# Optimization experiments

Measured on AMD Instinct MI355X. Metric: run time of the kernel, lower is better.

Reference implementation:

```python
import jax, jax.numpy as jnp
import numpy as np
from jax import lax

B, N, FIN, T, K, FC, FT = 8, 2048, 3, 12, 3, 64, 64


def _conv2d(x, w, b, pad):
    # x [B,C,N,T], w [O,I,1,kw], NCHW conv
    y = lax.conv_general_dilated(x, w, (1, 1), pad,
                                 dimension_numbers=('NCHW', 'OIHW', 'NCHW'))
    return y + b[None, :, None, None]


def _spatial_att(h, W, a, alpha, concat):
    # GAT-style dense attention. h [B,N,Fin], W [Fin,D], a [2D,1]
    D = W.shape[1]
    Wh = h @ W                                             # [B,N,D]
    e = jax.nn.leaky_relu(Wh @ a[:D] + jnp.swapaxes(Wh @ a[D:], 1, 2), alpha)  # [B,N,N]
    att = jax.nn.softmax(jax.nn.sigmoid(e), axis=1)        # softmax over dim=1 (as in torch)
    hp = jnp.einsum('bij,bjd->bid', att, Wh)
    return jax.nn.elu(hp) if concat else hp


def setup_inputs() -> dict:
    key = jax.random.key(0)
    ks = jax.random.split(key, 24)
    rnd = lambda i, shape, scale=1.0: (jax.random.normal(ks[i], shape, dtype=jnp.float32) * scale)
    FTm = FC * T  # 768 spatial-attention feature dim
    D = FTm // 2
    return {
        'x': rnd(0, (B, N, FIN, T)),
        'cheb': rnd(1, (K, N, N), 1.0 / np.sqrt(N)),
        'Gamma': rnd(2, (K, FIN, FC), 1.0 / np.sqrt(FIN)),
        'W_heads': rnd(3, (2, FTm, D), 1.0 / np.sqrt(FTm)),
        'a_heads': rnd(4, (2, 2 * D, 1), 1.0 / np.sqrt(2 * D)),
        'W_out': rnd(5, (FTm, FTm), 1.0 / np.sqrt(FTm)),
        'a_out': rnd(6, (2 * FTm, 1), 1.0 / np.sqrt(2 * FTm)),
        'U1': rnd(7, (FT, FT), 1.0 / np.sqrt(FT)),
        'U2': rnd(8, (FT,), 1.0 / np.sqrt(FT)),
        'U3': rnd(9, (FT,), 1.0 / np.sqrt(FT)),
        'be': rnd(10, (1, T, T), 0.1),
        'Ve': rnd(11, (T, T), 1.0 / np.sqrt(T)),
        'time_w': rnd(12, (FT, FC, 1, 3), 1.0 / np.sqrt(3 * FC)),
        'time_b': rnd(13, (FT,), 0.01),
        'res_w': rnd(14, (FT, FIN, 1, 1), 1.0 / np.sqrt(FIN)),
        'res_b': rnd(15, (FT,), 0.01),
        'back_w': rnd(16, (FT, FC, 1, 3), 1.0 / np.sqrt(3 * FC)),
        'back_b': rnd(17, (FT,), 0.01),
        'fore_w': rnd(18, (FT, FC, 1, 3), 1.0 / np.sqrt(3 * FC)),
        'fore_b': rnd(19, (FT,), 0.01),
        'ln_g': jnp.ones((FT,), jnp.float32),
        'ln_b': jnp.zeros((FT,), jnp.float32),
    }


def reference(x, cheb, Gamma, W_heads, a_heads, W_out, a_out, U1, U2, U3, be, Ve,
              time_w, time_b, res_w, res_b, back_w, back_b, fore_w, fore_b, ln_g, ln_b):
    b, n, fin, t = x.shape
    k_ = cheb.shape[0]
    fc = Gamma.shape[2]
    # ChebNetII interpolation coefficients T_k(x_j), x_j = cos((j+0.5)pi/K) -> [j,k]
    jj = np.arange(k_)
    cxj = jnp.asarray(np.cos(np.outer((jj + 0.5) * np.pi / k_, np.arange(k_))), x.dtype)
    lhs = jnp.einsum('jio,jk->kio', Gamma, cxj)                         # [K,Fin,Fc]
    rhs = jnp.einsum('bnit,knm->kbmit', x, cheb)                        # [K,B,N,Fin,T]
    spatial_gcn = jax.nn.relu((2.0 / (k_ + 1)) * jnp.einsum('kbmit,kio->bmot', rhs, lhs))  # [B,N,Fc,T]

    # Spatial transformer: 2 GAT heads + output attention
    h = spatial_gcn.reshape(b, n, fc * t)
    heads = jax.vmap(lambda W, a: _spatial_att(h, W, a, 0.1, True))(W_heads, a_heads)  # [H,B,N,D]
    hcat = jnp.transpose(heads, (1, 2, 0, 3)).reshape(b, n, -1)
    gcn_SAt = jax.nn.relu(_spatial_att(hcat, W_out, a_out, 0.1, False)).reshape(b, n, fc, t)

    # Temporal conv (1x3, pad 1)
    tc = _conv2d(jnp.transpose(gcn_SAt, (0, 2, 1, 3)), time_w, time_b, ((0, 0), (1, 1)))
    tc = jnp.transpose(tc, (0, 2, 1, 3))                                # [B,N,Ft,T]

    # Temporal attention
    lhs_t = jnp.einsum('bnft,fg,g->btn', tc, U1, U2)                    # [B,T,N]
    rhs_t = jnp.einsum('f,bnft->bnt', U3, tc)                           # [B,N,T]
    prod = jnp.einsum('bsn,bnt->bst', lhs_t, rhs_t)                     # [B,T,T]
    E = jnp.einsum('is,bst->bit', Ve, jax.nn.sigmoid(prod + be))
    E = jax.nn.softmax(E, axis=1)
    tcn = jnp.einsum('bnft,bts->bnfs', tc, E)                           # [B,N,Ft,T]

    # Residual (1x1 conv) + LayerNorm over channel dim
    x_res = _conv2d(jnp.transpose(x, (0, 2, 1, 3)), res_w, res_b, ((0, 0), (0, 0)))
    x_res = jnp.transpose(x_res, (0, 2, 1, 3))                          # [B,N,Ft,T]
    z = jnp.transpose(jax.nn.relu(x_res + tcn), (0, 3, 1, 2))           # [B,T,N,Ft]
    mu = z.mean(-1, keepdims=True)
    var = z.var(-1, keepdims=True)
    z = (z - mu) / jnp.sqrt(var + 1e-5) * ln_g + ln_b
    result = jnp.transpose(z, (0, 2, 3, 1))                             # [B,N,Ft,T]

    rp = jnp.transpose(result, (0, 2, 1, 3))
    backcast = jnp.transpose(_conv2d(rp, back_w, back_b, ((0, 0), (1, 1))), (0, 2, 1, 3))
    forecast = jnp.transpose(_conv2d(rp, fore_w, fore_b, ((0, 0), (1, 1))), (0, 2, 1, 3))
    return (backcast, forecast)
```

## Files before the change

kernel.cpp:

```cpp
#include <hip/hip_runtime.h>


typedef unsigned short u16;
typedef __bf16 bf16x8 __attribute__((ext_vector_type(8)));
typedef float f32x4 __attribute__((ext_vector_type(4)));
typedef u16 u16x8 __attribute__((ext_vector_type(8)));

__device__ __forceinline__ u16 f2b(float f) {
  union { float f; unsigned u; } v; v.f = f;
  unsigned u = v.u;
  u = u + 0x7FFFu + ((u >> 16) & 1u);
  return (u16)(u >> 16);
}
__device__ __forceinline__ float b2f(u16 h) {
  union { unsigned u; float f; } v; v.u = ((unsigned)h) << 16; return v.f;
}
__device__ __forceinline__ float qfun(float x) {
  float e = x > 0.f ? x : 0.1f * x;
  float s = __builtin_amdgcn_rcpf(1.f + __expf(-e));
  return __expf(s);
}

template <int N> __device__ __forceinline__ void waitvm() {
  if constexpr (N == 0)      asm volatile("s_waitcnt vmcnt(0)" ::: "memory");
  else if constexpr (N == 4) asm volatile("s_waitcnt vmcnt(4)" ::: "memory");
  else                       asm volatile("s_waitcnt vmcnt(6)" ::: "memory");
}
__device__ __forceinline__ void rawbar() { asm volatile("s_barrier" ::: "memory"); }

#define GLOAD16(g, l) __builtin_amdgcn_global_load_lds( \
    (__attribute__((address_space(1))) void*)(g),       \
    (__attribute__((address_space(3))) void*)(l), 16, 0, 0)

constexpr size_t OFF_LHS     = 0x0;
constexpr size_t OFF_U1U2    = 0x1000;
constexpr size_t OFF_BIASBIG = 0x1100;
constexpr size_t OFF_FH      = 0x3000;
constexpr size_t OFF_GH      = 0x23000;
constexpr size_t OFF_RDH     = 0x43000;
constexpr size_t OFF_FO      = 0x63000;
constexpr size_t OFF_GO      = 0x73000;
constexpr size_t OFF_RDO     = 0x83000;
constexpr size_t OFF_LHST    = 0x93000;
constexpr size_t OFF_RHST    = 0x153000;
constexpr size_t OFF_PROD    = 0x213000;
constexpr size_t OFF_E       = 0x215000;
constexpr size_t OFF_WCATT   = 0x220000;
constexpr size_t OFF_WOUTT   = 0x340000;
constexpr size_t OFF_WTBIG   = 0x460000;
constexpr size_t OFF_XCOLT   = 0x580000;
constexpr size_t OFF_CHEBT   = 0x700000;
constexpr size_t OFF_C1      = 0x1F00000;
constexpr size_t OFF_H       = 0x4300000;
constexpr size_t OFF_P       = 0x700000;
constexpr size_t OFF_WHCATT  = 0x5B00000;
constexpr size_t OFF_HCAT    = 0x7300000;
constexpr size_t OFF_WHOUTT  = 0x5B00000;
constexpr size_t OFF_GCNB    = 0x7300000;
constexpr size_t OFF_WBFBIG  = 0x8B00000;
constexpr size_t OFF_TCS     = 0x700000;
constexpr size_t OFF_RESULTB = 0x3700000;
constexpr size_t WS_NEEDED   = 0x8D40000;

struct GemmP {
  const u16* A; const u16* BT;
  long sA, sB;
  int K, lda, ldb;
  int swz, splitK;
  float* Cf; long sCf; int ldcf;
  u16* Cb;  long sCb; int ldcb;
  u16* CbT; int ldcT; long sCbT;
  const float* bias;
  float* outB; float* outF;
};

template <int EPI, int WN>
__global__ __launch_bounds__(256, (WN == 1 ? 3 : 2)) void gemm_bf16(GemmP p) {
  constexpr int BUFU  = (WN == 1) ? 8192 : 12288;
  constexpr int SMEMU = 3 * BUFU;
  constexpr int LPW   = (WN == 1) ? 4 : 6;
  __shared__ u16 smem[SMEMU];
  const int tid  = threadIdx.x;
  const int lane = tid & 63;
  const int wid  = tid >> 6;
  const int wm = wid >> 1, wn = wid & 1;
  const int z = blockIdx.z;

  long m0, n0;
  if (p.swz) {
    int nT = gridDim.x;
    int nwg = nT * gridDim.y;
    int lin = blockIdx.x + nT * blockIdx.y;
    int q = nwg >> 3;
    int swz = (lin & 7) * q + (lin >> 3);
    m0 = (long)(swz / nT) * 128;
    n0 = (long)(swz % nT) * (128 * WN);
  } else {
    m0 = (long)blockIdx.y * 128;
    n0 = (long)blockIdx.x * (128 * WN);
  }

  const int K = p.K;
  long aBase, bBase;
  if (p.splitK) {
    int kz = z >> 2, ch = z & 3;
    aBase = (long)kz * p.sA + (long)ch * 512;
    bBase = (long)ch * 512;
  } else {
    aBase = (long)z * p.sA;
    bBase = (long)z * p.sB;
  }
  const u16* Ab = p.A + aBase + m0 * p.lda;
  const u16* Bb = p.BT + bBase + n0 * p.ldb;

  const int sk = (((lane & 3) ^ ((lane >> 3) & 3))) * 8;
  const u16* aP0 = Ab + (long)(wid * 32 + (lane >> 2)) * p.lda + sk;
  const u16* aP1 = aP0 + (long)16 * p.lda;
  const u16* bP0 = Bb + (long)(wid * 32 * WN + (lane >> 2)) * p.ldb + sk;
  const u16* bP1 = bP0 + (long)16 * p.ldb;
  const u16* bP2 = bP0 + (long)32 * p.ldb;
  const u16* bP3 = bP0 + (long)48 * p.ldb;
  const int aslot = wid * 1024;
  const int bslot = 4096 + wid * (WN == 1 ? 1024 : 2048);

  auto STAGE = [&](int s, int bi) {
    long ko = (long)s * 32;
    u16* base = smem + bi * BUFU;
    GLOAD16(aP0 + ko, base + aslot);
    GLOAD16(aP1 + ko, base + aslot + 512);
    GLOAD16(bP0 + ko, base + bslot);
    GLOAD16(bP1 + ko, base + bslot + 512);
    if constexpr (WN == 2) {
      GLOAD16(bP2 + ko, base + bslot + 1024);
      GLOAD16(bP3 + ko, base + bslot + 1536);
    }
  };

  f32x4 acc[4][4 * WN];
  f32x4 zero = {0.f, 0.f, 0.f, 0.f};
#pragma unroll
  for (int i = 0; i < 4; ++i)
#pragma unroll
    for (int j = 0; j < 4 * WN; ++j) acc[i][j] = zero;

  const int xorc = (lane >> 1) & 3;
  const int aoff = (wm * 64 + (lane & 15)) * 32 + ((lane >> 4) ^ xorc) * 8;
  const int boff = 4096 + (wn * 64 * WN + (lane & 15)) * 32 + ((lane >> 4) ^ xorc) * 8;

  const int nsteps = K >> 5;

  STAGE(0, 0);
  STAGE(1, 1);
  waitvm<LPW>();
  rawbar();

  int cur = 0;
  for (int i = 0; i < nsteps; ++i) {
    const u16* buf = smem + cur * BUFU;
    bf16x8 av[4], bv[4 * WN];
#pragma unroll
    for (int mi = 0; mi < 4; ++mi) av[mi] = *(const bf16x8*)&buf[aoff + mi * 512];
#pragma unroll
    for (int ni = 0; ni < 4 * WN; ++ni) bv[ni] = *(const bf16x8*)&buf[boff + ni * 512];
#pragma unroll
    for (int mi = 0; mi < 4; ++mi)
#pragma unroll
      for (int ni = 0; ni < 4 * WN; ++ni)
        acc[mi][ni] = __builtin_amdgcn_mfma_f32_16x16x32_bf16(av[mi], bv[ni], acc[mi][ni], 0, 0, 0);
    if (i + 1 < nsteps) {
      if (i + 2 < nsteps) {
        STAGE(i + 2, cur == 0 ? 2 : cur - 1);
        waitvm<LPW>();
      } else {
        waitvm<0>();
      }
      rawbar();
    }
    cur = (cur == 2) ? 0 : cur + 1;
  }
  __syncthreads();

  if constexpr (EPI == 1) {
#pragma unroll
    for (int h = 0; h < 2; ++h) {
      if (h == 1) __syncthreads();
      if (WN == 1 || wn == h) {
#pragma unroll
        for (int mi = 0; mi < 4; ++mi)
#pragma unroll
          for (int ni = 0; ni < 4 * WN; ++ni) {
            int cl = (WN == 1 ? wn * 64 : 0) + ni * 16 + (lane & 15);
            int mlb = wm * 64 + mi * 16 + ((lane >> 4) << 2);
#pragma unroll
            for (int r = 0; r < 4; ++r)
              smem[cl * 136 + mlb + r] = f2b(acc[mi][ni][r]);
          }
      }
      __syncthreads();
      int c = tid >> 1, half = tid & 1;
      long bat = m0 >> 11;
      u16* dst = p.CbT + bat * p.sCbT + (long)(n0 + h * 128 + c) * p.ldcT +
                 (m0 & 2047) + half * 64;
      const u16* srcp = &smem[c * 136 + half * 64];
#pragma unroll
      for (int j = 0; j < 64; j += 8)
        *(u16x8*)(dst + j) = *(const u16x8*)(srcp + j);
      if (WN == 1) break;
    }
    return;
  }

  if constexpr (EPI == 7) {
    const int q = lane >> 4, g4 = (lane >> 2) & 3, j = lane & 3;
    const int back = ((int)n0 < 768);
    float* obase = (back ? p.outB : p.outF) - (back ? 0 : 768);
#pragma unroll
    for (int mi = 0; mi < 4; ++mi) {
      long rb0 = m0 + wm * 64 + mi * 16 + q * 4;
#pragma unroll
      for (int ni = 0; ni < 4 * WN; ++ni) {
        int cb = (int)n0 + wn * 64 * WN + ni * 16 + g4 * 4;
        f32x4 v = acc[mi][ni];
        float bsv = p.bias[cb + j];
        v[0] += bsv; v[1] += bsv; v[2] += bsv; v[3] += bsv;
#pragma unroll
        for (int d = 1; d <= 2; d <<= 1) {
          f32x4 t;
#pragma unroll
          for (int b = 0; b < 4; ++b) t[b] = __shfl_xor(v[b ^ d], d, 64);
#pragma unroll
          for (int b = 0; b < 4; ++b) if ((lane ^ b) & d) v[b] = t[b];
        }
        *(f32x4*)(obase + (rb0 + j) * 768 + cb) = v;
      }
    }
    return;
  }

#pragma unroll
  for (int mi = 0; mi < 4; ++mi) {
    long rb0 = m0 + wm * 64 + mi * 16 + ((lane >> 4) << 2);
#pragma unroll
    for (int ni = 0; ni < 4 * WN; ++ni) {
      int col = (int)n0 + wn * 64 * WN + ni * 16 + (lane & 15);
#pragma unroll
      for (int r = 0; r < 4; ++r) {
        float v = acc[mi][ni][r];
        long row = rb0 + r;
        if constexpr (EPI == 2) {
          float e = v > 0.f ? v : expm1f(v);
          p.Cb[(long)z * p.sCb + row * p.ldcb + col] = f2b(e);
        } else if constexpr (EPI == 6) {
          p.Cb[row * 768 + col] = f2b(v + p.bias[col & 63]);
        } else if constexpr (EPI == 9) {
          p.Cb[(long)z * p.sCb + row * p.ldcb + col] = f2b(v);
        } else {
          p.Cb[(long)z * p.sCb + row * p.ldcb + col] = f2b(fmaxf(v, 0.f));
        }
      }
    }
  }
}

__global__ void k_prep(const float* Gamma, const float* U1, const float* U2,
                       const float* back_b, const float* fore_b,
                       float* lhs, float* u1u2, float* biasBig) {
  int o = threadIdx.x;
  if (o < 64) {
    const float cx[3][3] = {{1.f, 0.86602540378443871f, 0.5f},
                            {1.f, 6.123233995736766e-17f, -1.f},
                            {1.f, -0.86602540378443871f, 0.5f}};
    for (int k = 0; k < 3; ++k)
      for (int i = 0; i < 3; ++i) {
        float s = 0;
        for (int j = 0; j < 3; ++j) s += Gamma[(j * 3 + i) * 64 + o] * cx[j][k];
        lhs[(k * 3 + i) * 64 + o] = s;
      }
    float s = 0;
    for (int g = 0; g < 64; ++g) s += U1[o * 64 + g] * U2[g];
    u1u2[o] = s;
    for (int t = 0; t < 12; ++t) {
      biasBig[o * 12 + t] = back_b[o];
      biasBig[768 + o * 12 + t] = fore_b[o];
    }
  }
}

__global__ void k_convert(const float* W_heads, const float* W_out, const float* time_w,
                          const float* back_w, const float* fore_w, const float* xg,
                          u16* WcatT, u16* WoutT, u16* WtBig, u16* WbfBig, u16* xcolT) {
  const int N1 = 589824, NT = 589824, NBF = 1179648, N5 = 786432;
  const int TOT = 2 * N1 + NT + NBF + N5;
  for (int o = blockIdx.x * 256 + threadIdx.x; o < TOT; o += gridDim.x * 256) {
    if (o < N1) {
      int dcol = o / 768, kk = o % 768;
      int hd = dcol / 384, d = dcol % 384;
      WcatT[o] = f2b(W_heads[((long)hd * 768 + kk) * 384 + d]);
    } else if (o < 2 * N1) {
      int o2 = o - N1; int dcol = o2 / 768, kk = o2 % 768;
      WoutT[o2] = f2b(W_out[kk * 768 + dcol]);
    } else if (o < 2 * N1 + NT) {
      int o3 = o - 2 * N1; int col = o3 / 768, kk = o3 % 768;
      int t = col >> 6, ft = col & 63, fc = kk / 12, tau = kk % 12;
      int r = tau - t + 1;
      WtBig[o3] = f2b((r >= 0 && r < 3) ? time_w[ft * 192 + fc * 3 + r] : 0.f);
    } else if (o < 2 * N1 + NT + NBF) {
      int o4 = o - 2 * N1 - NT; int col = o4 / 768, kk = o4 % 768;
      int rem = (col < 768) ? col : col - 768;
      int c = rem / 12, tt = rem % 12;
      int fc = kk / 12, tau = kk % 12; int r = tau - tt + 1;
      const float* wsrc = (col < 768) ? back_w : fore_w;
      WbfBig[o4] = f2b((r >= 0 && r < 3) ? wsrc[c * 192 + fc * 3 + r] : 0.f);
    } else {
      int o5 = o - 2 * N1 - NT - NBF; int c = o5 / 2048, n = o5 % 2048;
      float v = 0.f;
      if (c < 288) {
        int b = c / 36, r2 = c % 36, i = r2 / 12, t = r2 % 12;
        v = xg[(long)(b * 2048 + n) * 36 + i * 12 + t];
      }
      xcolT[o5] = f2b(v);
    }
  }
}

__global__ void k_chebT(const float* cheb, u16* chebT) {
  __shared__ float ts[32][33];
  int n0 = blockIdx.x * 32, m0 = blockIdx.y * 32, k = blockIdx.z;
  int c = threadIdx.x & 31, rq = threadIdx.x >> 5;
  const long base = (long)k * 2048 * 2048;
  for (int q = 0; q < 4; ++q) {
    int n = n0 + rq + q * 8;
    ts[rq + q * 8][c] = cheb[base + (long)n * 2048 + m0 + c];
  }
  __syncthreads();
  for (int q = 0; q < 4; ++q) {
    int m = m0 + rq + q * 8;
    chebT[base + (long)m * 2048 + n0 + c] = f2b(ts[c][rq + q * 8]);
  }
}

__global__ __launch_bounds__(256) void k_h(const u16* C1, const float* lhs, u16* h) {
  int bn = blockIdx.x; int b = bn >> 11, n = bn & 2047;
  int tid = threadIdx.x;
  __shared__ float c1s[108], ls[576];
  if (tid < 108) {
    int kk = tid / 12, t = tid % 12; int k = kk / 3, i = kk % 3;
    float s = 0;
#pragma unroll
    for (int ch = 0; ch < 4; ++ch)
      s += b2f(C1[((long)(k * 4 + ch) * 2048 + n) * 384 + b * 36 + i * 12 + t]);
    c1s[tid] = s;
  }
  for (int s = tid; s < 576; s += 256) ls[s] = lhs[s];
  __syncthreads();
  for (int q = 0; q < 3; ++q) {
    int idx = tid + q * 256; int o = idx / 12, t = idx % 12;
    float s = 0;
#pragma unroll
    for (int kk = 0; kk < 9; ++kk) s += c1s[kk * 12 + t] * ls[kk * 64 + o];
    s *= 0.5f;
    if (s < 0.f) s = 0.f;
    h[(long)bn * 768 + idx] = f2b(s);
  }
}

__global__ __launch_bounds__(256) void k_fg(const u16* WhT, int dOff, int Dlen,
                                            const float* aF, const float* aG,
                                            float* fOut, float* gOut) {
  int b = blockIdx.y;
  int i = blockIdx.x * 256 + threadIdx.x;
  __shared__ float af[768], ag[768];
  for (int s = threadIdx.x; s < Dlen; s += 256) { af[s] = aF[s]; ag[s] = aG[s]; }
  __syncthreads();
  const u16* wp = WhT + ((long)b * 768 + dOff) * 2048 + i;
  float fs = 0, gs = 0;
  for (int d = 0; d < Dlen; ++d) {
    float w = b2f(wp[(long)d * 2048]);
    fs += w * af[d]; gs += w * ag[d];
  }
  fOut[b * 2048 + i] = fs;
  gOut[b * 2048 + i] = gs;
}

__global__ __launch_bounds__(256) void k_denom(const float* f, const float* g, float* rd) {
  int b = blockIdx.y;
  int jl = threadIdx.x & 63, ch = threadIdx.x >> 6;
  int j = blockIdx.x * 64 + jl;
  __shared__ float fl[2048];
  __shared__ float red[256];
  for (int s = threadIdx.x; s < 2048; s += 256) fl[s] = f[b * 2048 + s];
  __syncthreads();
  float gj = g[b * 2048 + j];
  float acc = 0;
  for (int i = ch * 512; i < ch * 512 + 512; ++i) acc += qfun(fl[i] + gj);
  red[threadIdx.x] = acc;
  __syncthreads();
  if (ch == 0) {
    float s = red[jl] + red[jl + 64] + red[jl + 128] + red[jl + 192];
    rd[b * 2048 + j] = 1.f / s;
  }
}

__global__ __launch_bounds__(256) void k_P(const float* f, const float* g,
                                           const float* rd, u16* P) {
  int j = blockIdx.x * 256 + threadIdx.x;
  int i0 = blockIdx.y * 16;
  int b = blockIdx.z;
  __shared__ float fl[16];
  if (threadIdx.x < 16) fl[threadIdx.x] = f[b * 2048 + i0 + threadIdx.x];
  __syncthreads();
  float gj = g[b * 2048 + j], rj = rd[b * 2048 + j];
  u16* Pp = P + ((long)b * 2048 + i0) * 2048 + j;
#pragma unroll
  for (int ii = 0; ii < 16; ++ii) Pp[(long)ii * 2048] = f2b(qfun(fl[ii] + gj) * rj);
}

__global__ void k_temporal(const u16* tc, const float* u1u2, const float* U3g,
                           float* lhs_t, float* rhs_t) {
  __shared__ float uu[64], u3[64];
  int tid = threadIdx.x;
  if (tid < 64) { uu[tid] = u1u2[tid]; u3[tid] = U3g[tid]; }
  __syncthreads();
  int gid = blockIdx.x * 256 + tid;
  const u16* p = tc + (long)gid * 64;
  float s1 = 0, s2 = 0;
#pragma unroll
  for (int c = 0; c < 8; ++c) {
    u16x8 vv = *(const u16x8*)(p + c * 8);
#pragma unroll
    for (int j = 0; j < 8; ++j) {
      float v = b2f(vv[j]);
      s1 += v * uu[c * 8 + j]; s2 += v * u3[c * 8 + j];
    }
  }
  int t = gid % 12; long bn = gid / 12;
  int b = (int)(bn >> 11);
  lhs_t[((long)b * 12 + t) * 2048 + (int)(bn & 2047)] = s1;
  rhs_t[gid] = s2;
}

__global__ void k_prod(const float* lhs_t, const float* rhs_t, float* prod) {
  int bi = blockIdx.x;
  int b = bi / 144; int r = bi % 144; int s = r / 12; int u = r % 12;
  int tid = threadIdx.x;
  float acc = 0;
  const float* lp = lhs_t + ((long)b * 12 + s) * 2048;
  const float* rp = rhs_t + (long)b * 2048 * 12 + u;
  for (int n = tid; n < 2048; n += 256) acc += lp[n] * rp[n * 12];
  __shared__ float red[256];
  red[tid] = acc; __syncthreads();
  for (int st = 128; st > 0; st >>= 1) {
    if (tid < st) red[tid] += red[tid + st];
    __syncthreads();
  }
  if (tid == 0) prod[bi] = red[0];
}

__global__ void k_E(const float* prod, const float* be, const float* Ve, float* E) {
  int b = blockIdx.x; int tid = threadIdx.x;
  __shared__ float S0[144], E1[144], mx[12], dn[12];
  if (tid < 144) {
    float v = prod[b * 144 + tid] + be[tid];
    S0[tid] = 1.f / (1.f + __expf(-v));
  }
  __syncthreads();
  if (tid < 144) {
    int i = tid / 12, t = tid % 12;
    float a = 0;
    for (int s = 0; s < 12; ++s) a += Ve[i * 12 + s] * S0[s * 12 + t];
    E1[tid] = a;
  }
  __syncthreads();
  if (tid < 12) {
    float m = -1e30f;
    for (int i = 0; i < 12; ++i) m = fmaxf(m, E1[i * 12 + tid]);
    float d = 0;
    for (int i = 0; i < 12; ++i) d += __expf(E1[i * 12 + tid] - m);
    mx[tid] = m; dn[tid] = d;
  }
  __syncthreads();
  if (tid < 144) {
    int t = tid % 12;
    E[b * 144 + tid] = __expf(E1[tid] - mx[t]) / dn[t];
  }
}

__global__ __launch_bounds__(256) void k_res_ln(const u16* tc, const float* E,
                                                const float* xg, const float* res_w,
                                                const float* res_b, const float* ln_g,
                                                const float* ln_b, u16* result) {
  int bn = blockIdx.x; int b = bn >> 11;
  int tid = threadIdx.x;
  __shared__ float tcb[768], Eb[144], xl[36], rw[192], rb[64], lg[64], lb[64], zl[768], mu[12], rs[12];
  for (int s = tid; s < 768; s += 256) tcb[s] = b2f(tc[(long)bn * 768 + s]);
  if (tid < 144) Eb[tid] = E[b * 144 + tid];
  if (tid < 36) xl[tid] = xg[(long)bn * 36 + tid];
  if (tid >= 64 && tid < 256) { int q = tid - 64; if (q < 192) rw[q] = res_w[q]; }
  if (tid < 64) { rb[tid] = res_b[tid]; lg[tid] = ln_g[tid]; lb[tid] = ln_b[tid]; }
  __syncthreads();
  float z[3];
#pragma unroll
  for (int q = 0; q < 3; ++q) {
    int idx = tid + q * 256; int f = idx / 12, s = idx % 12;
    float tcn = 0;
#pragma unroll
    for (int t = 0; t < 12; ++t) tcn += tcb[t * 64 + f] * Eb[t * 12 + s];
    float xr = rb[f];
#pragma unroll
    for (int i = 0; i < 3; ++i) xr += rw[f * 3 + i] * xl[i * 12 + s];
    float v = xr + tcn;
    v = v > 0.f ? v : 0.f;
    z[q] = v; zl[idx] = v;
  }
  __syncthreads();
  if (tid < 12) {
    float m = 0, m2 = 0;
    for (int f = 0; f < 64; ++f) { float v = zl[f * 12 + tid]; m += v; m2 += v * v; }
    m *= (1.f / 64.f); m2 *= (1.f / 64.f);
    mu[tid] = m;
    float var = m2 - m * m;
    rs[tid] = rsqrtf((var > 0.f ? var : 0.f) + 1e-5f);
  }
  __syncthreads();
#pragma unroll
  for (int q = 0; q < 3; ++q) {
    int idx = tid + q * 256; int f = idx / 12, s = idx % 12;
    result[(long)bn * 768 + idx] = f2b((z[q] - mu[s]) * rs[s] * lg[f] + lb[f]);
  }
}

__global__ void k_sentinel(float* out, long n) {
  long i = (long)blockIdx.x * 256 + threadIdx.x;
  if (i < n) out[i] = 12345.0f;
}

extern "C" void kernel_launch(void* const* d_in, const int* in_sizes, int n_in,
                              void* d_out, int out_size, void* d_ws, size_t ws_size,
                              hipStream_t stream) {
  (void)in_sizes; (void)n_in;
  const float* x       = (const float*)d_in[0];
  const float* cheb    = (const float*)d_in[1];
  const float* Gamma   = (const float*)d_in[2];
  const float* W_heads = (const float*)d_in[3];
  const float* a_heads = (const float*)d_in[4];
  const float* W_out   = (const float*)d_in[5];
  const float* a_out   = (const float*)d_in[6];
  const float* U1      = (const float*)d_in[7];
  const float* U2      = (const float*)d_in[8];
  const float* U3      = (const float*)d_in[9];
  const float* be      = (const float*)d_in[10];
  const float* Ve      = (const float*)d_in[11];
  const float* time_w  = (const float*)d_in[12];
  const float* time_b  = (const float*)d_in[13];
  const float* res_w   = (const float*)d_in[14];
  const float* res_b   = (const float*)d_in[15];
  const float* back_w  = (const float*)d_in[16];
  const float* back_b  = (const float*)d_in[17];
  const float* fore_w  = (const float*)d_in[18];
  const float* fore_b  = (const float*)d_in[19];
  const float* ln_g    = (const float*)d_in[20];
  const float* ln_b    = (const float*)d_in[21];
  float* out = (float*)d_out;

  if (ws_size < WS_NEEDED) {
    k_sentinel<<<(out_size + 255) / 256, 256, 0, stream>>>(out, out_size);
    return;
  }

  char* ws = (char*)d_ws;
  float* lhs     = (float*)(ws + OFF_LHS);
  float* u1u2    = (float*)(ws + OFF_U1U2);
  float* biasBig = (float*)(ws + OFF_BIASBIG);
  float* fH      = (float*)(ws + OFF_FH);
  float* gH      = (float*)(ws + OFF_GH);
  float* rdH     = (float*)(ws + OFF_RDH);
  float* fO      = (float*)(ws + OFF_FO);
  float* gO      = (float*)(ws + OFF_GO);
  float* rdO     = (float*)(ws + OFF_RDO);
  float* lhs_t   = (float*)(ws + OFF_LHST);
  float* rhs_t   = (float*)(ws + OFF_RHST);
  float* prod    = (float*)(ws + OFF_PROD);
  float* Ebuf    = (float*)(ws + OFF_E);
  u16* WcatT   = (u16*)(ws + OFF_WCATT);
  u16* WoutT   = (u16*)(ws + OFF_WOUTT);
  u16* WtBig   = (u16*)(ws + OFF_WTBIG);
  u16* WbfBig  = (u16*)(ws + OFF_WBFBIG);
  u16* xcolT   = (u16*)(ws + OFF_XCOLT);
  u16* chebT   = (u16*)(ws + OFF_CHEBT);
  u16* C1      = (u16*)(ws + OFF_C1);
  u16* hbuf    = (u16*)(ws + OFF_H);
  u16* Pbuf    = (u16*)(ws + OFF_P);
  u16* WhcatT  = (u16*)(ws + OFF_WHCATT);
  u16* hcat    = (u16*)(ws + OFF_HCAT);
  u16* WhoutT  = (u16*)(ws + OFF_WHOUTT);
  u16* gcnB    = (u16*)(ws + OFF_GCNB);
  u16* tcsB    = (u16*)(ws + OFF_TCS);
  u16* resultB = (u16*)(ws + OFF_RESULTB);

  k_prep<<<1, 64, 0, stream>>>(Gamma, U1, U2, back_b, fore_b, lhs, u1u2, biasBig);
  k_convert<<<2048, 256, 0, stream>>>(W_heads, W_out, time_w, back_w, fore_w, x,
                                      WcatT, WoutT, WtBig, WbfBig, xcolT);
  k_chebT<<<dim3(64, 64, 3), 256, 0, stream>>>(cheb, chebT);

  {
    GemmP p{}; p.A = chebT; p.BT = xcolT; p.sA = 2048L * 2048; p.sB = 0;
    p.K = 512; p.lda = 2048; p.ldb = 2048; p.splitK = 1; p.swz = 1;
    p.Cb = C1; p.sCb = 2048L * 384; p.ldcb = 384;
    gemm_bf16<9, 1><<<dim3(3, 16, 12), 256, 0, stream>>>(p);
  }
  k_h<<<16384, 256, 0, stream>>>(C1, lhs, hbuf);

  {
    GemmP p{}; p.A = hbuf; p.BT = WcatT; p.sA = 0; p.sB = 0;
    p.K = 768; p.lda = 768; p.ldb = 768; p.swz = 1;
    p.CbT = WhcatT; p.ldcT = 2048; p.sCbT = 768L * 2048;
    gemm_bf16<1, 2><<<dim3(3, 128, 1), 256, 0, stream>>>(p);
  }
  k_fg<<<dim3(8, 8), 256, 0, stream>>>(WhcatT, 0, 384, a_heads, a_heads + 384, fH, gH);
  k_fg<<<dim3(8, 8), 256, 0, stream>>>(WhcatT, 384, 384, a_heads + 768, a_heads + 1152,
                                       fH + 16384, gH + 16384);
  for (int hd = 0; hd < 2; ++hd) {
    const float* f = fH + hd * 16384; const float* g = gH + hd * 16384;
    float* rd = rdH + hd * 16384;
    k_denom<<<dim3(32, 8), 256, 0, stream>>>(f, g, rd);
    k_P<<<dim3(8, 128, 8), 256, 0, stream>>>(f, g, rd, Pbuf);
    GemmP p{}; p.A = Pbuf; p.BT = WhcatT + (long)hd * 384 * 2048;
    p.sA = 2048L * 2048; p.sB = 768L * 2048;
    p.K = 2048; p.lda = 2048; p.ldb = 2048; p.swz = 1;
    p.Cb = hcat + hd * 384; p.sCb = 2048L * 768; p.ldcb = 768;
    gemm_bf16<2, 1><<<dim3(3, 16, 8), 256, 0, stream>>>(p);
  }

  {
    GemmP p{}; p.A = hcat; p.BT = WoutT; p.sA = 0; p.sB = 0;
    p.K = 768; p.lda = 768; p.ldb = 768; p.swz = 1;
    p.CbT = WhoutT; p.ldcT = 2048; p.sCbT = 768L * 2048;
    gemm_bf16<1, 2><<<dim3(3, 128, 1), 256, 0, stream>>>(p);
  }
  k_fg<<<dim3(8, 8), 256, 0, stream>>>(WhoutT, 0, 768, a_out, a_out + 768, fO, gO);
  k_denom<<<dim3(32, 8), 256, 0, stream>>>(fO, gO, rdO);
  k_P<<<dim3(8, 128, 8), 256, 0, stream>>>(fO, gO, rdO, Pbuf);
  {
    GemmP p{}; p.A = Pbuf; p.BT = WhoutT; p.sA = 2048L * 2048; p.sB = 768L * 2048;
    p.K = 2048; p.lda = 2048; p.ldb = 2048; p.swz = 1;
    p.Cb = gcnB; p.sCb = 2048L * 768; p.ldcb = 768;
    gemm_bf16<8, 2><<<dim3(3, 16, 8), 256, 0, stream>>>(p);
  }

  {
    GemmP p{}; p.A = gcnB; p.BT = WtBig; p.sA = 0; p.sB = 0;
    p.K = 768; p.lda = 768; p.ldb = 768; p.swz = 1;
    p.Cb = tcsB; p.bias = time_b;
    gemm_bf16<6, 2><<<dim3(3, 128, 1), 256, 0, stream>>>(p);
  }

  k_temporal<<<768, 256, 0, stream>>>(tcsB, u1u2, U3, lhs_t, rhs_t);
  k_prod<<<1152, 256, 0, stream>>>(lhs_t, rhs_t, prod);
  k_E<<<8, 256, 0, stream>>>(prod, be, Ve, Ebuf);

  k_res_ln<<<16384, 256, 0, stream>>>(tcsB, Ebuf, x, res_w, res_b, ln_g, ln_b, resultB);

  {
    GemmP p{}; p.A = resultB; p.BT = WbfBig; p.sA = 0; p.sB = 0;
    p.K = 768; p.lda = 768; p.ldb = 768; p.swz = 1;
    p.bias = biasBig; p.outB = out; p.outF = out + 12582912L;
    gemm_bf16<7, 2><<<dim3(6, 128, 1), 256, 0, stream>>>(p);
  }
}
```

Baseline: 702.8 us.

## Write attention matrix in MFMA fragment layout and load A directly to registers

The attention-probability kernel now writes P in pre-swizzled MFMA fragment order, 16-row by 32-k tiles with 8 contiguous bf16 values per lane. The P-times-Wh GEMMs gain an AF mode that reads A fragments straight from global memory into registers, double-buffered across two steps, and stage only B through LDS. This removes LDS traffic and shared-memory footprint for the large A operand and vectorises the P stores. The cost is more outstanding vector-memory loads per wave and register pressure from keeping prefetched A fragments.

```diff
diff --git a/kernel.cpp b/kernel.cpp
--- a/kernel.cpp
+++ b/kernel.cpp
@@ -23,8 +23,10 @@
 
 template <int N> __device__ __forceinline__ void waitvm() {
   if constexpr (N == 0)      asm volatile("s_waitcnt vmcnt(0)" ::: "memory");
+  else if constexpr (N == 2) asm volatile("s_waitcnt vmcnt(2)" ::: "memory");
   else if constexpr (N == 4) asm volatile("s_waitcnt vmcnt(4)" ::: "memory");
-  else                       asm volatile("s_waitcnt vmcnt(6)" ::: "memory");
+  else if constexpr (N == 6) asm volatile("s_waitcnt vmcnt(6)" ::: "memory");
+  else                       asm volatile("s_waitcnt vmcnt(8)" ::: "memory");
 }
 __device__ __forceinline__ void rawbar() { asm volatile("s_barrier" ::: "memory"); }
 
@@ -74,11 +76,12 @@
   float* outB; float* outF;
 };
 
-template <int EPI, int WN>
+template <int EPI, int WN, int AF = 0>
 __global__ __launch_bounds__(256, (WN == 1 ? 3 : 2)) void gemm_bf16(GemmP p) {
-  constexpr int BUFU  = (WN == 1) ? 8192 : 12288;
+  constexpr int BUFU  = AF ? (WN == 1 ? 4096 : 8192) : (WN == 1 ? 8192 : 12288);
   constexpr int SMEMU = 3 * BUFU;
-  constexpr int LPW   = (WN == 1) ? 4 : 6;
+  constexpr int LPWB  = AF ? (WN == 1 ? 2 : 4) : (WN == 1 ? 4 : 6);
+  constexpr int WVN   = AF ? (LPWB + 4) : LPWB;
   __shared__ u16 smem[SMEMU];
   const int tid  = threadIdx.x;
   const int lane = tid & 63;
@@ -121,13 +124,15 @@
   const u16* bP2 = bP0 + (long)32 * p.ldb;
   const u16* bP3 = bP0 + (long)48 * p.ldb;
   const int aslot = wid * 1024;
-  const int bslot = 4096 + wid * (WN == 1 ? 1024 : 2048);
+  const int bslot = (AF ? 0 : 4096) + wid * (WN == 1 ? 1024 : 2048);
 
   auto STAGE = [&](int s, int bi) {
     long ko = (long)s * 32;
     u16* base = smem + bi * BUFU;
-    GLOAD16(aP0 + ko, base + aslot);
-    GLOAD16(aP1 + ko, base + aslot + 512);
+    if constexpr (!AF) {
+      GLOAD16(aP0 + ko, base + aslot);
+      GLOAD16(aP1 + ko, base + aslot + 512);
+    }
     GLOAD16(bP0 + ko, base + bslot);
     GLOAD16(bP1 + ko, base + bslot + 512);
     if constexpr (WN == 2) {
@@ -145,38 +150,80 @@
 
   const int xorc = (lane >> 1) & 3;
   const int aoff = (wm * 64 + (lane & 15)) * 32 + ((lane >> 4) ^ xorc) * 8;
-  const int boff = 4096 + (wn * 64 * WN + (lane & 15)) * 32 + ((lane >> 4) ^ xorc) * 8;
+  const int boff = (AF ? 0 : 4096) + (wn * 64 * WN + (lane & 15)) * 32 + ((lane >> 4) ^ xorc) * 8;
 
   const int nsteps = K >> 5;
-
-  STAGE(0, 0);
-  STAGE(1, 1);
-  waitvm<LPW>();
-  rawbar();
-
   int cur = 0;
-  for (int i = 0; i < nsteps; ++i) {
-    const u16* buf = smem + cur * BUFU;
-    bf16x8 av[4], bv[4 * WN];
-#pragma unroll
-    for (int mi = 0; mi < 4; ++mi) av[mi] = *(const bf16x8*)&buf[aoff + mi * 512];
-#pragma unroll
-    for (int ni = 0; ni < 4 * WN; ++ni) bv[ni] = *(const bf16x8*)&buf[boff + ni * 512];
-#pragma unroll
-    for (int mi = 0; mi < 4; ++mi)
-#pragma unroll
-      for (int ni = 0; ni < 4 * WN; ++ni)
-        acc[mi][ni] = __builtin_amdgcn_mfma_f32_16x16x32_bf16(av[mi], bv[ni], acc[mi][ni], 0, 0, 0);
-    if (i + 1 < nsteps) {
-      if (i + 2 < nsteps) {
-        STAGE(i + 2, cur == 0 ? 2 : cur - 1);
-        waitvm<LPW>();
-      } else {
-        waitvm<0>();
+
+  if constexpr (AF) {
+    const long kt512 = (long)(K >> 5) * 512;
+    const u16* aPf = p.A + (long)z * p.sA + ((m0 >> 4) + wm * 4) * kt512 + lane * 8;
+    bf16x8 avA[4], avB[4];
+#pragma unroll
+    for (int mi = 0; mi < 4; ++mi) avA[mi] = *(const bf16x8*)(aPf + mi * kt512);
+    STAGE(0, 0);
+#pragma unroll
+    for (int mi = 0; mi < 4; ++mi) avB[mi] = *(const bf16x8*)(aPf + mi * kt512 + 512);
+    STAGE(1, 1);
+    waitvm<WVN>();
+    rawbar();
+
+    auto STEPAF = [&](int i, bf16x8 (&av)[4]) {
+      const u16* buf = smem + cur * BUFU;
+      bf16x8 bv[4 * WN];
+#pragma unroll
+      for (int ni = 0; ni < 4 * WN; ++ni) bv[ni] = *(const bf16x8*)&buf[boff + ni * 512];
+#pragma unroll
+      for (int mi = 0; mi < 4; ++mi)
+#pragma unroll
+        for (int ni = 0; ni < 4 * WN; ++ni)
+          acc[mi][ni] = __builtin_amdgcn_mfma_f32_16x16x32_bf16(av[mi], bv[ni], acc[mi][ni], 0, 0, 0);
+      if (i + 1 < nsteps) {
+        if (i + 2 < nsteps) {
+          STAGE(i + 2, cur == 0 ? 2 : cur - 1);
+#pragma unroll
+          for (int mi = 0; mi < 4; ++mi)
+            av[mi] = *(const bf16x8*)(aPf + mi * kt512 + (long)(i + 2) * 512);
+          waitvm<WVN>();
+        } else {
+          waitvm<0>();
+        }
+        rawbar();
       }
-      rawbar();
-    }
-    cur = (cur == 2) ? 0 : cur + 1;
+      cur = (cur == 2) ? 0 : cur + 1;
+    };
+    for (int i = 0; i < nsteps; i += 2) {
+      STEPAF(i, avA);
+      if (i + 1 < nsteps) STEPAF(i + 1, avB);
+    }
+  } else {
+    STAGE(0, 0);
+    STAGE(1, 1);
+    waitvm<WVN>();
+    rawbar();
+    for (int i = 0; i < nsteps; ++i) {
+      const u16* buf = smem + cur * BUFU;
+      bf16x8 av[4], bv[4 * WN];
+#pragma unroll
+      for (int mi = 0; mi < 4; ++mi) av[mi] = *(const bf16x8*)&buf[aoff + mi * 512];
+#pragma unroll
+      for (int ni = 0; ni < 4 * WN; ++ni) bv[ni] = *(const bf16x8*)&buf[boff + ni * 512];
+#pragma unroll
+      for (int mi = 0; mi < 4; ++mi)
+#pragma unroll
+        for (int ni = 0; ni < 4 * WN; ++ni)
+          acc[mi][ni] = __builtin_amdgcn_mfma_f32_16x16x32_bf16(av[mi], bv[ni], acc[mi][ni], 0, 0, 0);
+      if (i + 1 < nsteps) {
+        if (i + 2 < nsteps) {
+          STAGE(i + 2, cur == 0 ? 2 : cur - 1);
+          waitvm<WVN>();
+        } else {
+          waitvm<0>();
+        }
+        rawbar();
+      }
+      cur = (cur == 2) ? 0 : cur + 1;
+    }
   }
   __syncthreads();
 
@@ -401,18 +448,30 @@
   }
 }
 
-__global__ __launch_bounds__(256) void k_P(const float* f, const float* g,
-                                           const float* rd, u16* P) {
-  int j = blockIdx.x * 256 + threadIdx.x;
-  int i0 = blockIdx.y * 16;
-  int b = blockIdx.z;
-  __shared__ float fl[16];
-  if (threadIdx.x < 16) fl[threadIdx.x] = f[b * 2048 + i0 + threadIdx.x];
-  __syncthreads();
-  float gj = g[b * 2048 + j], rj = rd[b * 2048 + j];
-  u16* Pp = P + ((long)b * 2048 + i0) * 2048 + j;
-#pragma unroll
-  for (int ii = 0; ii < 16; ++ii) Pp[(long)ii * 2048] = f2b(qfun(fl[ii] + gj) * rj);
+__global__ __launch_bounds__(256) void k_Pfrag(const float* f, const float* g,
+                                               const float* rd, u16* P) {
+  int z = blockIdx.z, mt = blockIdx.y;
+  int wid = threadIdx.x >> 6, lane = threadIdx.x & 63;
+  int kt = blockIdx.x * 4 + wid;
+  const float* fb = f + z * 2048;
+  const float* gb = g + z * 2048;
+  const float* rb = rd + z * 2048;
+  float fv = fb[mt * 16 + (lane & 15)];
+  int k0 = kt * 32 + (lane >> 4) * 8;
+  float4 g0 = *(const float4*)(gb + k0);
+  float4 g1 = *(const float4*)(gb + k0 + 4);
+  float4 r0 = *(const float4*)(rb + k0);
+  float4 r1 = *(const float4*)(rb + k0 + 4);
+  u16x8 o;
+  o[0] = f2b(qfun(fv + g0.x) * r0.x);
+  o[1] = f2b(qfun(fv + g0.y) * r0.y);
+  o[2] = f2b(qfun(fv + g0.z) * r0.z);
+  o[3] = f2b(qfun(fv + g0.w) * r0.w);
+  o[4] = f2b(qfun(fv + g1.x) * r1.x);
+  o[5] = f2b(qfun(fv + g1.y) * r1.y);
+  o[6] = f2b(qfun(fv + g1.z) * r1.z);
+  o[7] = f2b(qfun(fv + g1.w) * r1.w);
+  *(u16x8*)(P + (long)z * 4194304 + ((long)(mt * 64 + kt)) * 512 + lane * 8) = o;
 }
 
 __global__ void k_temporal(const u16* tc, const float* u1u2, const float* U3g,
@@ -623,12 +682,12 @@
     const float* f = fH + hd * 16384; const float* g = gH + hd * 16384;
     float* rd = rdH + hd * 16384;
     k_denom<<<dim3(32, 8), 256, 0, stream>>>(f, g, rd);
-    k_P<<<dim3(8, 128, 8), 256, 0, stream>>>(f, g, rd, Pbuf);
+    k_Pfrag<<<dim3(16, 128, 8), 256, 0, stream>>>(f, g, rd, Pbuf);
     GemmP p{}; p.A = Pbuf; p.BT = WhcatT + (long)hd * 384 * 2048;
     p.sA = 2048L * 2048; p.sB = 768L * 2048;
     p.K = 2048; p.lda = 2048; p.ldb = 2048; p.swz = 1;
     p.Cb = hcat + hd * 384; p.sCb = 2048L * 768; p.ldcb = 768;
-    gemm_bf16<2, 1><<<dim3(3, 16, 8), 256, 0, stream>>>(p);
+    gemm_bf16<2, 1, 1><<<dim3(3, 16, 8), 256, 0, stream>>>(p);
   }
 
   {
@@ -639,12 +698,12 @@
   }
   k_fg<<<dim3(8, 8), 256, 0, stream>>>(WhoutT, 0, 768, a_out, a_out + 768, fO, gO);
   k_denom<<<dim3(32, 8), 256, 0, stream>>>(fO, gO, rdO);
-  k_P<<<dim3(8, 128, 8), 256, 0, stream>>>(fO, gO, rdO, Pbuf);
+  k_Pfrag<<<dim3(16, 128, 8), 256, 0, stream>>>(fO, gO, rdO, Pbuf);
   {
     GemmP p{}; p.A = Pbuf; p.BT = WhoutT; p.sA = 2048L * 2048; p.sB = 768L * 2048;
     p.K = 2048; p.lda = 2048; p.ldb = 2048; p.swz = 1;
     p.Cb = gcnB; p.sCb = 2048L * 768; p.ldcb = 768;
-    gemm_bf16<8, 2><<<dim3(3, 16, 8), 256, 0, stream>>>(p);
+    gemm_bf16<8, 2, 1><<<dim3(3, 16, 8), 256, 0, stream>>>(p);
   }
 
   {
```

Result: no change. 713.1 us (+1.5%).

## Store GEMM operands in MFMA-fragment order and load them directly to registers

Applied to the files above, without the earlier changes.

Adds a new GEMM kernel that reads A and B operands straight from global memory into registers, skipping LDS staging. This works because the producers (k_h, k_res_ln and the weight conversion) now write their outputs pre-tiled in the 16x32 MFMA fragment layout. The kernel uses a three-stage register software pipeline and 128x128 tiles, and is applied to the Wh projection and the backcast/forecast GEMMs. It removes LDS traffic and barriers, but raises register pressure and relies on L2 for data reuse across waves.

```diff
diff --git a/kernel.cpp b/kernel.cpp
--- a/kernel.cpp
+++ b/kernel.cpp
@@ -24,7 +24,8 @@
 template <int N> __device__ __forceinline__ void waitvm() {
   if constexpr (N == 0)      asm volatile("s_waitcnt vmcnt(0)" ::: "memory");
   else if constexpr (N == 4) asm volatile("s_waitcnt vmcnt(4)" ::: "memory");
-  else                       asm volatile("s_waitcnt vmcnt(6)" ::: "memory");
+  else if constexpr (N == 6) asm volatile("s_waitcnt vmcnt(6)" ::: "memory");
+  else                       asm volatile("s_waitcnt vmcnt(16)" ::: "memory");
 }
 __device__ __forceinline__ void rawbar() { asm volatile("s_barrier" ::: "memory"); }
 
@@ -74,6 +75,114 @@
   float* outB; float* outF;
 };
 
+template <int EPI>
+__global__ __launch_bounds__(256, 2) void gemm_afb(GemmP p) {
+  __shared__ u16 smem[(EPI == 1) ? 17408 : 16];
+  const int tid = threadIdx.x, lane = tid & 63, wid = tid >> 6;
+  const int wm = wid >> 1, wn = wid & 1;
+  const int z = blockIdx.z;
+  int nT = gridDim.x;
+  int nwg = nT * gridDim.y;
+  int lin = blockIdx.x + nT * blockIdx.y;
+  int q8 = nwg >> 3;
+  int sw = (lin & 7) * q8 + (lin >> 3);
+  long m0 = (long)(sw / nT) * 128;
+  long n0 = (long)(sw % nT) * 128;
+
+  const int KT = p.K >> 5;
+  const long mstr = (long)KT * 512;
+  const u16* aPf = p.A + (long)z * p.sA + ((m0 >> 4) + wm * 4) * mstr + lane * 8;
+  const u16* bPf = p.BT + ((n0 >> 4) + wn * 4) * mstr + lane * 8;
+
+  f32x4 acc[4][4];
+  f32x4 zero = {0.f, 0.f, 0.f, 0.f};
+#pragma unroll
+  for (int i = 0; i < 4; ++i)
+#pragma unroll
+    for (int j = 0; j < 4; ++j) acc[i][j] = zero;
+
+  bf16x8 a0[4], b0[4], a1[4], b1[4], a2[4], b2[4];
+  auto LOAD = [&](bf16x8 (&av)[4], bf16x8 (&bv)[4], int s) {
+#pragma unroll
+    for (int mi = 0; mi < 4; ++mi) av[mi] = *(const bf16x8*)(aPf + mi * mstr + (long)s * 512);
+#pragma unroll
+    for (int ni = 0; ni < 4; ++ni) bv[ni] = *(const bf16x8*)(bPf + ni * mstr + (long)s * 512);
+  };
+  auto MM = [&](bf16x8 (&av)[4], bf16x8 (&bv)[4]) {
+#pragma unroll
+    for (int mi = 0; mi < 4; ++mi)
+#pragma unroll
+      for (int ni = 0; ni < 4; ++ni)
+        acc[mi][ni] = __builtin_amdgcn_mfma_f32_16x16x32_bf16(av[mi], bv[ni], acc[mi][ni], 0, 0, 0);
+  };
+
+  LOAD(a0, b0, 0);
+  if (KT > 1) LOAD(a1, b1, 1);
+  if (KT > 2) LOAD(a2, b2, 2);
+  for (int i = 0; i < KT; i += 3) {
+    waitvm<16>(); MM(a0, b0);
+    if (i + 3 < KT) LOAD(a0, b0, i + 3);
+    if (i + 1 < KT) {
+      waitvm<16>(); MM(a1, b1);
+      if (i + 4 < KT) LOAD(a1, b1, i + 4);
+    }
+    if (i + 2 < KT) {
+      waitvm<16>(); MM(a2, b2);
+      if (i + 5 < KT) LOAD(a2, b2, i + 5);
+    }
+  }
+
+  if constexpr (EPI == 1) {
+    __syncthreads();
+#pragma unroll
+    for (int mi = 0; mi < 4; ++mi)
+#pragma unroll
+      for (int ni = 0; ni < 4; ++ni) {
+        int cl = wn * 64 + ni * 16 + (lane & 15);
+        int mlb = wm * 64 + mi * 16 + ((lane >> 4) << 2);
+#pragma unroll
+        for (int r = 0; r < 4; ++r)
+          smem[cl * 136 + mlb + r] = f2b(acc[mi][ni][r]);
+      }
+    __syncthreads();
+    int c = tid >> 1, half = tid & 1;
+    long bat = m0 >> 11;
+    u16* dst = p.CbT + bat * p.sCbT + (long)(n0 + c) * p.ldcT + (m0 & 2047) + half * 64;
+    const u16* srcp = &smem[c * 136 + half * 64];
+#pragma unroll
+    for (int j = 0; j < 64; j += 8)
+      *(u16x8*)(dst + j) = *(const u16x8*)(srcp + j);
+    return;
+  }
+
+  if constexpr (EPI == 7) {
+    const int q = lane >> 4, g4 = (lane >> 2) & 3, j = lane & 3;
+    const int back = ((int)n0 < 768);
+    float* obase = (back ? p.outB : p.outF) - (back ? 0 : 768);
+#pragma unroll
+    for (int mi = 0; mi < 4; ++mi) {
+      long rb0 = m0 + wm * 64 + mi * 16 + q * 4;
+#pragma unroll
+      for (int ni = 0; ni < 4; ++ni) {
+        int cb = (int)n0 + wn * 64 + ni * 16 + g4 * 4;
+        f32x4 v = acc[mi][ni];
+        float bsv = p.bias[cb + j];
+        v[0] += bsv; v[1] += bsv; v[2] += bsv; v[3] += bsv;
+#pragma unroll
+        for (int d = 1; d <= 2; d <<= 1) {
+          f32x4 t;
+#pragma unroll
+          for (int b = 0; b < 4; ++b) t[b] = __shfl_xor(v[b ^ d], d, 64);
+#pragma unroll
+          for (int b = 0; b < 4; ++b) if ((lane ^ b) & d) v[b] = t[b];
+        }
+        *(f32x4*)(obase + (rb0 + j) * 768 + cb) = v;
+      }
+    }
+    return;
+  }
+}
+
 template <int EPI, int WN>
 __global__ __launch_bounds__(256, (WN == 1 ? 3 : 2)) void gemm_bf16(GemmP p) {
   constexpr int BUFU  = (WN == 1) ? 8192 : 12288;
@@ -206,33 +315,6 @@
       for (int j = 0; j < 64; j += 8)
         *(u16x8*)(dst + j) = *(const u16x8*)(srcp + j);
       if (WN == 1) break;
-    }
-    return;
-  }
-
-  if constexpr (EPI == 7) {
-    const int q = lane >> 4, g4 = (lane >> 2) & 3, j = lane & 3;
-    const int back = ((int)n0 < 768);
-    float* obase = (back ? p.outB : p.outF) - (back ? 0 : 768);
-#pragma unroll
-    for (int mi = 0; mi < 4; ++mi) {
-      long rb0 = m0 + wm * 64 + mi * 16 + q * 4;
-#pragma unroll
-      for (int ni = 0; ni < 4 * WN; ++ni) {
-        int cb = (int)n0 + wn * 64 * WN + ni * 16 + g4 * 4;
-        f32x4 v = acc[mi][ni];
-        float bsv = p.bias[cb + j];
-        v[0] += bsv; v[1] += bsv; v[2] += bsv; v[3] += bsv;
-#pragma unroll
-        for (int d = 1; d <= 2; d <<= 1) {
-          f32x4 t;
-#pragma unroll
-          for (int b = 0; b < 4; ++b) t[b] = __shfl_xor(v[b ^ d], d, 64);
-#pragma unroll
-          for (int b = 0; b < 4; ++b) if ((lane ^ b) & d) v[b] = t[b];
-        }
-        *(f32x4*)(obase + (rb0 + j) * 768 + cb) = v;
-      }
     }
     return;
   }
@@ -293,7 +375,11 @@
   const int TOT = 2 * N1 + NT + NBF + N5;
   for (int o = blockIdx.x * 256 + threadIdx.x; o < TOT; o += gridDim.x * 256) {
     if (o < N1) {
-      int dcol = o / 768, kk = o % 768;
+      int f = o >> 9, s = o & 511;
+      int ln = s >> 3, j = s & 7;
+      int nf = f / 24, kt = f % 24;
+      int dcol = nf * 16 + (ln & 15);
+      int kk = kt * 32 + (ln >> 4) * 8 + j;
       int hd = dcol / 384, d = dcol % 384;
       WcatT[o] = f2b(W_heads[((long)hd * 768 + kk) * 384 + d]);
     } else if (o < 2 * N1) {
@@ -305,7 +391,12 @@
       int r = tau - t + 1;
       WtBig[o3] = f2b((r >= 0 && r < 3) ? time_w[ft * 192 + fc * 3 + r] : 0.f);
     } else if (o < 2 * N1 + NT + NBF) {
-      int o4 = o - 2 * N1 - NT; int col = o4 / 768, kk = o4 % 768;
+      int o4 = o - 2 * N1 - NT;
+      int f = o4 >> 9, s = o4 & 511;
+      int ln = s >> 3, j = s & 7;
+      int nf = f / 24, kt = f % 24;
+      int col = nf * 16 + (ln & 15);
+      int kk = kt * 32 + (ln >> 4) * 8 + j;
       int rem = (col < 768) ? col : col - 768;
       int c = rem / 12, tt = rem % 12;
       int fc = kk / 12, tau = kk % 12; int r = tau - tt + 1;
@@ -353,6 +444,7 @@
   }
   for (int s = tid; s < 576; s += 256) ls[s] = lhs[s];
   __syncthreads();
+  const int mf = bn >> 4, m = bn & 15;
   for (int q = 0; q < 3; ++q) {
     int idx = tid + q * 256; int o = idx / 12, t = idx % 12;
     float s = 0;
@@ -360,7 +452,8 @@
     for (int kk = 0; kk < 9; ++kk) s += c1s[kk * 12 + t] * ls[kk * 64 + o];
     s *= 0.5f;
     if (s < 0.f) s = 0.f;
-    h[(long)bn * 768 + idx] = f2b(s);
+    int kt = idx >> 5, koct = (idx >> 3) & 3, j = idx & 7;
+    h[((long)mf * 24 + kt) * 512 + (m + 16 * koct) * 8 + j] = f2b(s);
   }
 }
 
@@ -522,10 +615,13 @@
     rs[tid] = rsqrtf((var > 0.f ? var : 0.f) + 1e-5f);
   }
   __syncthreads();
+  const int mf = bn >> 4, m = bn & 15;
 #pragma unroll
   for (int q = 0; q < 3; ++q) {
     int idx = tid + q * 256; int f = idx / 12, s = idx % 12;
-    result[(long)bn * 768 + idx] = f2b((z[q] - mu[s]) * rs[s] * lg[f] + lb[f]);
+    int kt = idx >> 5, koct = (idx >> 3) & 3, j = idx & 7;
+    result[((long)mf * 24 + kt) * 512 + (m + 16 * koct) * 8 + j] =
+        f2b((z[q] - mu[s]) * rs[s] * lg[f] + lb[f]);
   }
 }
 
@@ -611,10 +707,9 @@
   k_h<<<16384, 256, 0, stream>>>(C1, lhs, hbuf);
 
   {
-    GemmP p{}; p.A = hbuf; p.BT = WcatT; p.sA = 0; p.sB = 0;
-    p.K = 768; p.lda = 768; p.ldb = 768; p.swz = 1;
+    GemmP p{}; p.A = hbuf; p.BT = WcatT; p.sA = 0; p.K = 768;
     p.CbT = WhcatT; p.ldcT = 2048; p.sCbT = 768L * 2048;
-    gemm_bf16<1, 2><<<dim3(3, 128, 1), 256, 0, stream>>>(p);
+    gemm_afb<1><<<dim3(6, 128, 1), 256, 0, stream>>>(p);
   }
   k_fg<<<dim3(8, 8), 256, 0, stream>>>(WhcatT, 0, 384, a_heads, a_heads + 384, fH, gH);
   k_fg<<<dim3(8, 8), 256, 0, stream>>>(WhcatT, 384, 384, a_heads + 768, a_heads + 1152,
@@ -661,9 +756,8 @@
   k_res_ln<<<16384, 256, 0, stream>>>(tcsB, Ebuf, x, res_w, res_b, ln_g, ln_b, resultB);
 
   {
-    GemmP p{}; p.A = resultB; p.BT = WbfBig; p.sA = 0; p.sB = 0;
-    p.K = 768; p.lda = 768; p.ldb = 768; p.swz = 1;
+    GemmP p{}; p.A = resultB; p.BT = WbfBig; p.sA = 0; p.K = 768;
     p.bias = biasBig; p.outB = out; p.outF = out + 12582912L;
-    gemm_bf16<7, 2><<<dim3(6, 128, 1), 256, 0, stream>>>(p);
-  }
-}
+    gemm_afb<7><<<dim3(12, 128, 1), 256, 0, stream>>>(p);
+  }
+}
```

New measurement: 701.0 us, median of 2. About the same (-0.3%).
